# Optimization experiments

Hardware: AMD Instinct MI355X
Metric: run time of the kernel (lower is better)

## Reference

```python
import jax, jax.numpy as jnp
from jax import lax
import numpy as np

B, CIN, H, W = 32, 256, 56, 56
BOTTLE, GROWTH = 128, 32
EPS = 1e-5
QMAX = 127.0  # 8-bit symmetric


def _fq(x, scale, qmax=QMAX):
    # fake-quantize with straight-through estimator
    q = jnp.clip(jnp.round(x / scale), -qmax - 1.0, qmax) * scale
    return x + lax.stop_gradient(q - x)


def fake_quant_act(x):
    # per-tensor symmetric 8-bit activation quantization (QuantAct)
    scale = lax.stop_gradient(jnp.max(jnp.abs(x)) / QMAX + 1e-8)
    return _fq(x, scale), scale


def quant_weight_pc(w):
    # per-output-channel symmetric 8-bit weight quantization, w: [O,I,kh,kw]
    scale = lax.stop_gradient(jnp.max(jnp.abs(w), axis=(1, 2, 3)) / QMAX + 1e-8)
    return _fq(w, scale[:, None, None, None]), scale


def conv2d(x, w, pad):
    return lax.conv_general_dilated(
        x, w, window_strides=(1, 1), padding=[(pad, pad), (pad, pad)],
        dimension_numbers=("NCHW", "OIHW", "NCHW"))


def setup_inputs() -> dict:
    key = jax.random.key(0)
    ks = jax.random.split(key, 12)
    return {
        "batch": jax.random.normal(ks[0], (B, CIN, H, W), jnp.float32),
        "input_scaling_factor": jnp.float32(0.05),
        "bn1_gamma": jax.random.uniform(ks[1], (CIN,), jnp.float32, 0.5, 1.5),
        "bn1_beta": jax.random.normal(ks[2], (CIN,), jnp.float32) * 0.1,
        "bn1_mean": jax.random.normal(ks[3], (CIN,), jnp.float32) * 0.1,
        "bn1_var": jax.random.uniform(ks[4], (CIN,), jnp.float32, 0.5, 1.5),
        "conv1_w": jax.random.normal(ks[5], (BOTTLE, CIN, 1, 1), jnp.float32) * 0.05,
        "bn2_gamma": jax.random.uniform(ks[6], (BOTTLE,), jnp.float32, 0.5, 1.5),
        "bn2_beta": jax.random.normal(ks[7], (BOTTLE,), jnp.float32) * 0.1,
        "bn2_mean": jax.random.normal(ks[8], (BOTTLE,), jnp.float32) * 0.1,
        "bn2_var": jax.random.uniform(ks[9], (BOTTLE,), jnp.float32, 0.5, 1.5),
        "conv2_w": jax.random.normal(ks[10], (GROWTH, BOTTLE, 3, 3), jnp.float32) * 0.05,
    }


def reference(batch, input_scaling_factor, bn1_gamma, bn1_beta, bn1_mean,
              bn1_var, conv1_w, bn2_gamma, bn2_beta, bn2_mean, bn2_var,
              conv2_w):
    s_in = input_scaling_factor
    # ---- QuantBn1: BN with fake-quantized folded weight/bias ----
    w1 = bn1_gamma * lax.rsqrt(bn1_var + EPS)            # [CIN]
    b1 = bn1_beta - bn1_mean * w1                        # [CIN]
    s_bn = lax.stop_gradient(jnp.max(jnp.abs(w1)) / QMAX + 1e-8)
    w1q = _fq(w1, s_bn)
    b1q = _fq(b1, s_in * s_bn, qmax=2.0 ** 31)           # bias quantized at s_in*s_w
    x = batch * w1q[None, :, None, None] + b1q[None, :, None, None]
    x = jax.nn.relu(x)                                   # act1
    x, s_a1 = fake_quant_act(x)                          # quant_act1
    # ---- QuantBnConv2d: fold bn2 into conv1 (1x1), per-channel weight quant ----
    t = bn2_gamma * lax.rsqrt(bn2_var + EPS)             # [BOTTLE]
    wf = conv1_w * t[:, None, None, None]
    bf = bn2_beta - bn2_mean * t
    wfq, s_w1 = quant_weight_pc(wf)                      # s_w1: [BOTTLE]
    bfq = _fq(bf, s_a1 * s_w1, qmax=2.0 ** 31)
    x = conv2d(x, wfq, pad=0) + bfq[None, :, None, None]
    x = jax.nn.relu(x)                                   # act2
    x, s_a2 = fake_quant_act(x)                          # quant_act2
    # ---- QuantConv2d: 3x3 growth conv, per-channel weight quant ----
    w2q, s_w2 = quant_weight_pc(conv2_w)
    x = conv2d(x, w2q, pad=1)                            # [B, GROWTH, H, W]
    # ---- concat + output requant ----
    cat = jnp.concatenate([batch, x], axis=1)            # [B, CIN+GROWTH, H, W]
    out, s_out = fake_quant_act(cat)                     # quant_act_output
    return out, s_out
```

## Files before the change

kernel.cpp:

```cpp
#include <hip/hip_runtime.h>

typedef __attribute__((ext_vector_type(8))) short bf16x8;
typedef __attribute__((ext_vector_type(4))) float f32x4;

constexpr int B_   = 32;
constexpr int CIN  = 256;
constexpr int HW   = 56 * 56;
constexpr int BOT  = 128;
constexpr int GRW  = 32;
constexpr int COUT = CIN + GRW;
constexpr int NBATCH = B_ * CIN * HW;
constexpr int NX2    = B_ * BOT * HW;
constexpr int NOUT   = B_ * COUT * HW;

constexpr int NSLOT = 32;
constexpr int SSTR  = 32;
constexpr int OFF_SLOT = 16;
constexpr int OFF_W1Q  = OFF_SLOT + 4 * NSLOT * SSTR;
constexpr int OFF_B1Q  = OFF_W1Q + 256;
constexpr int OFF_BFQ  = OFF_B1Q + 256;
constexpr int OFF_SC1  = OFF_BFQ + 128;
constexpr int OFF_SC2  = OFF_SC1 + 128;
constexpr int OFF_WQ1B = OFF_SC2 + 32;
constexpr int OFF_W2B  = OFF_WQ1B + 16384;
constexpr int OFF_END  = OFF_W2B + 18432;
constexpr size_t X1Q_BYTE = (size_t)OFF_END * 4;
constexpr size_t X2_BYTE  = X1Q_BYTE + (size_t)NBATCH;
constexpr size_t X3_BYTE  = X2_BYTE + (size_t)NX2 * 4;
constexpr size_t X2B_BYTE = X3_BYTE + (size_t)(B_ * GRW * HW) * 4;

__device__ __forceinline__ void slotAtomicMax(float* ws, int a, int s, float v) {
    atomicMax((unsigned*)ws + OFF_SLOT + a * NSLOT * SSTR + s * SSTR, __float_as_uint(v));
}
__device__ __forceinline__ float slotMax(const float* ws, int a) {
    float m = 0.0f;
    #pragma unroll
    for (int s = 0; s < NSLOT; s++)
        m = fmaxf(m, ws[OFF_SLOT + a * NSLOT * SSTR + s * SSTR]);
    return m;
}

__device__ __forceinline__ float blockReduceMax256(float v) {
    #pragma unroll
    for (int o = 32; o > 0; o >>= 1) v = fmaxf(v, __shfl_down(v, o, 64));
    __shared__ float sm[4];
    if ((threadIdx.x & 63) == 0) sm[threadIdx.x >> 6] = v;
    __syncthreads();
    return fmaxf(fmaxf(sm[0], sm[1]), fmaxf(sm[2], sm[3]));
}
__device__ __forceinline__ float waveReduceMax(float v) {
    #pragma unroll
    for (int o = 32; o > 0; o >>= 1) v = fmaxf(v, __shfl_down(v, o, 64));
    return v;
}
__device__ __forceinline__ float clamp8(float r)   { return fminf(fmaxf(r, -128.0f), 127.0f); }
__device__ __forceinline__ float clampBig(float r) { return fminf(fmaxf(r, -2147483648.0f), 2147483648.0f); }
__device__ __forceinline__ unsigned short bf16u(float f) { return (unsigned short)(__float_as_uint(f) >> 16); }

__global__ void prep1_kernel(const float* __restrict__ g1, const float* __restrict__ b1p,
                             const float* __restrict__ m1, const float* __restrict__ v1,
                             const float* __restrict__ s_in_p, float* __restrict__ ws) {
    int c = threadIdx.x;
    unsigned* scal = (unsigned*)ws;
    for (int s = c; s < OFF_W1Q; s += 256) scal[s] = 0u;
    float s_in = *s_in_p;
    float r = 1.0f / sqrtf(v1[c] + 1e-5f);
    float w1 = __fmul_rn(g1[c], r);
    float b1 = __fsub_rn(b1p[c], __fmul_rn(m1[c], w1));
    float mx = blockReduceMax256(fabsf(w1));
    float s_bn = mx / 127.0f + 1e-8f;
    ws[OFF_W1Q + c] = __fmul_rn(clamp8(rintf(w1 / s_bn)), s_bn);
    float sb = __fmul_rn(s_in, s_bn);
    ws[OFF_B1Q + c] = __fmul_rn(clampBig(rintf(b1 / sb)), sb);
}

__global__ __launch_bounds__(256) void max1_kernel(const float4* __restrict__ batch4,
                                                   float* __restrict__ ws) {
    const float* w1q = ws + OFF_W1Q;
    const float* b1q = ws + OFF_B1Q;
    int tid = blockIdx.x * 256 + threadIdx.x;
    int row = tid >> 4;
    int f   = tid & 15;
    int c   = row & 255;
    float w = w1q[c], b = b1q[c];
    const float4* p = batch4 + (size_t)row * 784 + f;
    float mx1 = 0.0f, mxb = 0.0f;
    #pragma unroll 7
    for (int k = 0; k < 49; k++) {
        float4 v = p[k * 16];
        float x0 = fmaxf(__fadd_rn(__fmul_rn(v.x, w), b), 0.0f);
        float x1 = fmaxf(__fadd_rn(__fmul_rn(v.y, w), b), 0.0f);
        float x2 = fmaxf(__fadd_rn(__fmul_rn(v.z, w), b), 0.0f);
        float x3 = fmaxf(__fadd_rn(__fmul_rn(v.w, w), b), 0.0f);
        mx1 = fmaxf(mx1, fmaxf(fmaxf(x0, x1), fmaxf(x2, x3)));
        mxb = fmaxf(mxb, fmaxf(fmaxf(fabsf(v.x), fabsf(v.y)), fmaxf(fabsf(v.z), fabsf(v.w))));
    }
    mx1 = blockReduceMax256(mx1);
    __syncthreads();
    mxb = blockReduceMax256(mxb);
    if (threadIdx.x == 0) {
        int s = blockIdx.x & (NSLOT - 1);
        slotAtomicMax(ws, 0, s, mx1);
        slotAtomicMax(ws, 1, s, mxb);
    }
}

__global__ __launch_bounds__(256) void quant1_kernel(const float4* __restrict__ batch4,
                                                     float* __restrict__ ws) {
    __shared__ unsigned ldsq[256 * 17];
    const float* w1q = ws + OFF_W1Q;
    const float* b1q = ws + OFF_B1Q;
    float s_a1 = slotMax(ws, 0) / 127.0f + 1e-8f;
    int b = blockIdx.x / 49, hw0 = (blockIdx.x % 49) * 64;
    int t = threadIdx.x;
    int f = t & 15, cb = t >> 4;
    #pragma unroll
    for (int j = 0; j < 16; j++) {
        int c = cb + j * 16;
        float w = w1q[c], bb = b1q[c];
        float4 v = batch4[(b * 256 + c) * 784 + (hw0 >> 2) + f];
        unsigned q0 = (unsigned)(int)clamp8(rintf(fmaxf(__fadd_rn(__fmul_rn(v.x, w), bb), 0.0f) / s_a1));
        unsigned q1 = (unsigned)(int)clamp8(rintf(fmaxf(__fadd_rn(__fmul_rn(v.y, w), bb), 0.0f) / s_a1));
        unsigned q2 = (unsigned)(int)clamp8(rintf(fmaxf(__fadd_rn(__fmul_rn(v.z, w), bb), 0.0f) / s_a1));
        unsigned q3 = (unsigned)(int)clamp8(rintf(fmaxf(__fadd_rn(__fmul_rn(v.w, w), bb), 0.0f) / s_a1));
        ldsq[c * 17 + f] = q0 | (q1 << 8) | (q2 << 16) | (q3 << 24);
    }
    __syncthreads();
    const unsigned char* l8 = (const unsigned char*)ldsq;
    uint4* outv = (uint4*)((char*)ws + X1Q_BYTE);
    int hwl = t >> 2, cq = (t & 3) * 16;
    #pragma unroll
    for (int k = 0; k < 4; k++) {
        int c0 = cq + k * 64;
        unsigned u[4] = {0u, 0u, 0u, 0u};
        #pragma unroll
        for (int i = 0; i < 16; i++) {
            unsigned by = l8[(c0 + i) * 68 + hwl];
            u[i >> 2] |= by << ((i & 3) * 8);
        }
        uint4 val; val.x = u[0]; val.y = u[1]; val.z = u[2]; val.w = u[3];
        outv[(((size_t)b * 3136 + hw0 + hwl) * 256 + c0) >> 4] = val;
    }
}

__global__ void prep2_kernel(const float* __restrict__ c1w,
                             const float* __restrict__ g2, const float* __restrict__ b2,
                             const float* __restrict__ m2, const float* __restrict__ v2,
                             const float* __restrict__ c2w, float* __restrict__ ws) {
    int bi = blockIdx.x;
    int t = threadIdx.x;
    unsigned short* wq1b = (unsigned short*)(ws + OFF_WQ1B);
    unsigned short* w2b  = (unsigned short*)(ws + OFF_W2B);
    if (bi < BOT) {
        int o = bi;
        float tt = __fmul_rn(g2[o], 1.0f / sqrtf(v2[o] + 1e-5f));
        float wf = __fmul_rn(c1w[o * CIN + t], tt);
        float mx = blockReduceMax256(fabsf(wf));
        float s_w1 = mx / 127.0f + 1e-8f;
        float m = clamp8(rintf(wf / s_w1));
        wq1b[o * CIN + t] = bf16u(m);
        if (t == 0) {
            float s_a1 = slotMax(ws, 0) / 127.0f + 1e-8f;
            ws[OFF_SC1 + o] = __fmul_rn(s_a1, s_w1);
            float bf = __fsub_rn(b2[o], __fmul_rn(m2[o], tt));
            float sb = __fmul_rn(s_a1, s_w1);
            ws[OFF_BFQ + o] = __fmul_rn(clampBig(rintf(bf / sb)), sb);
        }
    } else {
        int g = bi - BOT;
        float mx = 0.0f;
        for (int s = t; s < BOT * 9; s += 256) mx = fmaxf(mx, fabsf(c2w[g * BOT * 9 + s]));
        mx = blockReduceMax256(mx);
        float s_w2 = mx / 127.0f + 1e-8f;
        for (int s = t; s < BOT * 9; s += 256) {
            int c = s / 9, tap = s - c * 9;
            float m = clamp8(rintf(c2w[g * BOT * 9 + s] / s_w2));
            w2b[(tap * GRW + g) * BOT + c] = bf16u(m);
        }
        if (t == 0) ws[OFF_SC2 + g] = s_w2;
    }
}

__global__ __launch_bounds__(256) void conv1_kernel(float* __restrict__ ws) {
    __shared__ unsigned short lA[64 * 136];
    __shared__ unsigned short lW[128 * 136];
    __shared__ float wred[4];
    const unsigned char* x1q = (const unsigned char*)((char*)ws + X1Q_BYTE);
    const unsigned short* wq1b = (const unsigned short*)(ws + OFF_WQ1B);
    const float* sc1 = ws + OFF_SC1;
    const float* bfq = ws + OFF_BFQ;
    float* x2 = (float*)((char*)ws + X2_BYTE);
    int b = blockIdx.x / 49, hw0 = (blockIdx.x % 49) * 64;
    int t = threadIdx.x, lane = t & 63, wv = t >> 6;
    int quad = lane >> 4, l16 = lane & 15;
    int mhalf = wv & 1, nhalf = wv >> 1;
    f32x4 acc[2][4];
    #pragma unroll
    for (int i = 0; i < 2; i++)
        #pragma unroll
        for (int j = 0; j < 4; j++) acc[i][j] = (f32x4){0.f, 0.f, 0.f, 0.f};

    for (int kc = 0; kc < 256; kc += 128) {
        __syncthreads();
        {
            int cb = t & 7, hwi = t >> 3;
            #pragma unroll
            for (int r = 0; r < 2; r++) {
                int hw = hwi + r * 32;
                uint4 p = *(const uint4*)(x1q + ((size_t)b * 3136 + hw0 + hw) * 256 + kc + cb * 16);
                unsigned wd[4] = {p.x, p.y, p.z, p.w};
                bf16x8 t0, t1;
                #pragma unroll
                for (int j = 0; j < 8; j++)
                    t0[j] = (short)bf16u((float)((wd[j >> 2] >> ((j & 3) * 8)) & 255u));
                #pragma unroll
                for (int j = 0; j < 8; j++)
                    t1[j] = (short)bf16u((float)((wd[2 + (j >> 2)] >> ((j & 3) * 8)) & 255u));
                *(bf16x8*)&lA[hw * 136 + cb * 16] = t0;
                *(bf16x8*)&lA[hw * 136 + cb * 16 + 8] = t1;
            }
        }
        {
            int cb = t & 7, oi = t >> 3;
            #pragma unroll
            for (int r = 0; r < 4; r++) {
                int o = oi + r * 32;
                uint4 p0 = *(const uint4*)(wq1b + o * 256 + kc + cb * 16);
                uint4 p1 = *(const uint4*)(wq1b + o * 256 + kc + cb * 16 + 8);
                *(uint4*)&lW[o * 136 + cb * 16] = p0;
                *(uint4*)&lW[o * 136 + cb * 16 + 8] = p1;
            }
        }
        __syncthreads();
        #pragma unroll
        for (int ks = 0; ks < 4; ks++) {
            bf16x8 a0 = *(const bf16x8*)&lA[(mhalf * 32 + l16) * 136 + ks * 32 + quad * 8];
            bf16x8 a1 = *(const bf16x8*)&lA[(mhalf * 32 + 16 + l16) * 136 + ks * 32 + quad * 8];
            #pragma unroll
            for (int nt = 0; nt < 4; nt++) {
                bf16x8 bfr = *(const bf16x8*)&lW[(nhalf * 64 + nt * 16 + l16) * 136 + ks * 32 + quad * 8];
                acc[0][nt] = __builtin_amdgcn_mfma_f32_16x16x32_bf16(a0, bfr, acc[0][nt], 0, 0, 0);
                acc[1][nt] = __builtin_amdgcn_mfma_f32_16x16x32_bf16(a1, bfr, acc[1][nt], 0, 0, 0);
            }
        }
    }
    float mx = 0.0f;
    #pragma unroll
    for (int nt = 0; nt < 4; nt++) {
        int o = nhalf * 64 + nt * 16 + l16;
        float s = sc1[o], bb = bfq[o];
        #pragma unroll
        for (int mt = 0; mt < 2; mt++) {
            int hw = hw0 + mhalf * 32 + mt * 16 + quad * 4;
            float4 v;
            v.x = fmaxf(__fadd_rn(__fmul_rn(acc[mt][nt][0], s), bb), 0.0f);
            v.y = fmaxf(__fadd_rn(__fmul_rn(acc[mt][nt][1], s), bb), 0.0f);
            v.z = fmaxf(__fadd_rn(__fmul_rn(acc[mt][nt][2], s), bb), 0.0f);
            v.w = fmaxf(__fadd_rn(__fmul_rn(acc[mt][nt][3], s), bb), 0.0f);
            mx = fmaxf(mx, fmaxf(fmaxf(v.x, v.y), fmaxf(v.z, v.w)));
            *(float4*)&x2[(size_t)(b * BOT + o) * HW + hw] = v;
        }
    }
    mx = waveReduceMax(mx);
    if (lane == 0) wred[wv] = mx;
    __syncthreads();
    if (t == 0) {
        float m = fmaxf(fmaxf(wred[0], wred[1]), fmaxf(wred[2], wred[3]));
        slotAtomicMax(ws, 2, blockIdx.x & (NSLOT - 1), m);
    }
}

__global__ __launch_bounds__(256) void quant2_kernel(float* __restrict__ ws) {
    __shared__ unsigned short lt[128 * 66];
    unsigned short* x2b = (unsigned short*)((char*)ws + X2B_BYTE);
    int b = blockIdx.x / 58, hp = blockIdx.x % 58;
    int t = threadIdx.x;
    uint4* dst = (uint4*)(x2b + (size_t)(b * 58 + hp) * 8192);
    if (hp == 0 || hp == 57) {
        uint4 z; z.x = z.y = z.z = z.w = 0u;
        #pragma unroll
        for (int k = 0; k < 4; k++) dst[t + k * 256] = z;
        return;
    }
    int h = hp - 1;
    float s_a2 = slotMax(ws, 2) / 127.0f + 1e-8f;
    float rinv = 1.0f / s_a2;
    const float4* x24 = (const float4*)((char*)ws + X2_BYTE);
    unsigned* ltw = (unsigned*)lt;
    int f = t & 15, cb = t >> 4;
    if (f < 14) {
        #pragma unroll
        for (int j = 0; j < 8; j++) {
            int c = cb + j * 16;
            float4 v = x24[((size_t)b * 128 + c) * 784 + h * 14 + f];
            unsigned q0 = bf16u(clamp8(rintf(v.x * rinv)));
            unsigned q1 = bf16u(clamp8(rintf(v.y * rinv)));
            unsigned q2 = bf16u(clamp8(rintf(v.z * rinv)));
            unsigned q3 = bf16u(clamp8(rintf(v.w * rinv)));
            ltw[c * 33 + f * 2]     = q0 | (q1 << 16);
            ltw[c * 33 + f * 2 + 1] = q2 | (q3 << 16);
        }
    }
    __syncthreads();
    #pragma unroll
    for (int k = 0; k < 4; k++) {
        int idx = t + k * 256;
        int cblk = idx & 15, wp = idx >> 4;
        unsigned u[4] = {0u, 0u, 0u, 0u};
        if (wp >= 1 && wp <= 56) {
            #pragma unroll
            for (int i = 0; i < 8; i++) {
                unsigned s = lt[(cblk * 8 + i) * 66 + (wp - 1)];
                u[i >> 1] |= s << ((i & 1) * 16);
            }
        }
        uint4 val; val.x = u[0]; val.y = u[1]; val.z = u[2]; val.w = u[3];
        dst[wp * 16 + cblk] = val;
    }
}

__global__ __launch_bounds__(256) void conv2_kernel(float* __restrict__ ws) {
    __shared__ unsigned short wt[9 * 32 * 40];
    __shared__ float wred[4];
    const unsigned short* x2b = (const unsigned short*)((char*)ws + X2B_BYTE);
    const unsigned short* w2b = (const unsigned short*)(ws + OFF_W2B);
    const float* sc2 = ws + OFF_SC2;
    float* x3 = (float*)((char*)ws + X3_BYTE);
    int b = blockIdx.x / 28, hg = blockIdx.x % 28;
    int t = threadIdx.x, lane = t & 63, wv = t >> 6;
    int quad = lane >> 4, l16 = lane & 15;
    int h = hg * 2 + (wv >> 1);
    int wq = wv & 1;
    int w0 = wq * 24;
    float s_a2 = slotMax(ws, 2) / 127.0f + 1e-8f;

    const unsigned short* rowp[2][3];
    #pragma unroll
    for (int mt = 0; mt < 2; mt++) {
        int w = w0 + mt * 16 + l16;
        #pragma unroll
        for (int dh = 0; dh < 3; dh++)
            rowp[mt][dh] = x2b + ((size_t)(b * 58 + h + dh) * 64 + w) * 128 + quad * 8;
    }
    f32x4 acc[2][2];
    #pragma unroll
    for (int i = 0; i < 2; i++) { acc[i][0] = (f32x4){0.f,0.f,0.f,0.f}; acc[i][1] = (f32x4){0.f,0.f,0.f,0.f}; }

    for (int cs = 0; cs < 4; cs++) {
        __syncthreads();
        for (int s = t; s < 1152; s += 256) {
            int gi = s >> 2, q = s & 3;
            *(uint4*)&wt[gi * 40 + q * 8] = *(const uint4*)(w2b + gi * 128 + cs * 32 + q * 8);
        }
        __syncthreads();
        #pragma unroll
        for (int tap = 0; tap < 9; tap++) {
            int dh = tap / 3, dw = tap % 3;
            bf16x8 b0 = *(const bf16x8*)&wt[(tap * 32 + l16) * 40 + quad * 8];
            bf16x8 b1 = *(const bf16x8*)&wt[(tap * 32 + 16 + l16) * 40 + quad * 8];
            #pragma unroll
            for (int mt = 0; mt < 2; mt++) {
                bf16x8 a = *(const bf16x8*)(rowp[mt][dh] + dw * 128 + cs * 32);
                acc[mt][0] = __builtin_amdgcn_mfma_f32_16x16x32_bf16(a, b0, acc[mt][0], 0, 0, 0);
                acc[mt][1] = __builtin_amdgcn_mfma_f32_16x16x32_bf16(a, b1, acc[mt][1], 0, 0, 0);
            }
        }
    }
    float mx = 0.0f;
    #pragma unroll
    for (int nt = 0; nt < 2; nt++) {
        int g = nt * 16 + l16;
        float s2 = __fmul_rn(s_a2, sc2[g]);
        #pragma unroll
        for (int mt = 0; mt < 2; mt++) {
            int wb = w0 + mt * 16 + quad * 4;
            if (wq == 0 || wb >= 32) {
                float4 v;
                v.x = __fmul_rn(acc[mt][nt][0], s2);
                v.y = __fmul_rn(acc[mt][nt][1], s2);
                v.z = __fmul_rn(acc[mt][nt][2], s2);
                v.w = __fmul_rn(acc[mt][nt][3], s2);
                mx = fmaxf(mx, fmaxf(fmaxf(fabsf(v.x), fabsf(v.y)), fmaxf(fabsf(v.z), fabsf(v.w))));
                *(float4*)&x3[(size_t)(b * GRW + g) * HW + h * 56 + wb] = v;
            }
        }
    }
    mx = waveReduceMax(mx);
    if (lane == 0) wred[wv] = mx;
    __syncthreads();
    if (t == 0) {
        float m = fmaxf(fmaxf(wred[0], wred[1]), fmaxf(wred[2], wred[3]));
        slotAtomicMax(ws, 3, blockIdx.x & (NSLOT - 1), m);
    }
}

__global__ __launch_bounds__(256) void outq_kernel(const float4* __restrict__ batch4,
                                                   const float* __restrict__ ws,
                                                   float* __restrict__ out) {
    const float4* x34 = (const float4*)((const char*)ws + X3_BYTE);
    float maxb = slotMax(ws, 1);
    float max3 = slotMax(ws, 3);
    float s_out = fmaxf(maxb, max3) / 127.0f + 1e-8f;
    float4* out4 = (float4*)out;
    int n4 = NOUT / 4;
    for (int i = blockIdx.x * blockDim.x + threadIdx.x; i < n4; i += gridDim.x * blockDim.x) {
        int chl = i / 784;
        int b = chl / COUT;
        int ch = chl - b * COUT;
        int hw4 = i - chl * 784;
        float4 v;
        if (ch < CIN) v = batch4[(b * CIN + ch) * 784 + hw4];
        else          v = x34[(b * GRW + (ch - CIN)) * 784 + hw4];
        float4 r;
        r.x = __fmul_rn(clamp8(rintf(v.x / s_out)), s_out);
        r.y = __fmul_rn(clamp8(rintf(v.y / s_out)), s_out);
        r.z = __fmul_rn(clamp8(rintf(v.z / s_out)), s_out);
        r.w = __fmul_rn(clamp8(rintf(v.w / s_out)), s_out);
        out4[i] = r;
    }
    if (blockIdx.x == 0 && threadIdx.x == 0) out[NOUT] = s_out;
}

extern "C" void kernel_launch(void* const* d_in, const int* in_sizes, int n_in,
                              void* d_out, int out_size, void* d_ws, size_t ws_size,
                              hipStream_t stream) {
    const float* batch = (const float*)d_in[0];
    const float* s_in  = (const float*)d_in[1];
    const float* g1    = (const float*)d_in[2];
    const float* b1    = (const float*)d_in[3];
    const float* m1    = (const float*)d_in[4];
    const float* v1    = (const float*)d_in[5];
    const float* c1w   = (const float*)d_in[6];
    const float* g2    = (const float*)d_in[7];
    const float* b2    = (const float*)d_in[8];
    const float* m2    = (const float*)d_in[9];
    const float* v2    = (const float*)d_in[10];
    const float* c2w   = (const float*)d_in[11];
    float* out = (float*)d_out;
    float* ws  = (float*)d_ws;

    hipLaunchKernelGGL(prep1_kernel, dim3(1), dim3(256), 0, stream, g1, b1, m1, v1, s_in, ws);
    hipLaunchKernelGGL(max1_kernel, dim3(512), dim3(256), 0, stream, (const float4*)batch, ws);
    hipLaunchKernelGGL(quant1_kernel, dim3(32 * 49), dim3(256), 0, stream, (const float4*)batch, ws);
    hipLaunchKernelGGL(prep2_kernel, dim3(160), dim3(256), 0, stream, c1w, g2, b2, m2, v2, c2w, ws);
    hipLaunchKernelGGL(conv1_kernel, dim3(32 * 49), dim3(256), 0, stream, ws);
    hipLaunchKernelGGL(quant2_kernel, dim3(32 * 58), dim3(256), 0, stream, ws);
    hipLaunchKernelGGL(conv2_kernel, dim3(32 * 28), dim3(256), 0, stream, ws);
    hipLaunchKernelGGL(outq_kernel, dim3(4096), dim3(256), 0, stream, (const float4*)batch, ws, out);
}
```

Measured before the change: 345.3 us.

## Fuse act2 quantization into conv2 loads and write padded NHWC fp32 from conv1

conv1 now writes its post-ReLU fp32 output directly into a zero-padded channels-last buffer, and a small kernel zeroes the halo. The separate quant2 pass that transposed and quantized x2 to bf16 is removed, and conv2 quantizes on the fly as it loads fp32 activations. This drops one kernel launch and a full read plus write of the intermediate. In exchange conv2 reads fp32 (twice the bytes of bf16) nine times per element through global memory, and conv1's stores become scattered scalar writes.

```diff
diff --git a/kernel.cpp b/kernel.cpp
--- a/kernel.cpp
+++ b/kernel.cpp
@@ -10,7 +10,6 @@
 constexpr int GRW  = 32;
 constexpr int COUT = CIN + GRW;
 constexpr int NBATCH = B_ * CIN * HW;
-constexpr int NX2    = B_ * BOT * HW;
 constexpr int NOUT   = B_ * COUT * HW;
 
 constexpr int NSLOT = 32;
@@ -25,9 +24,9 @@
 constexpr int OFF_W2B  = OFF_WQ1B + 16384;
 constexpr int OFF_END  = OFF_W2B + 18432;
 constexpr size_t X1Q_BYTE = (size_t)OFF_END * 4;
-constexpr size_t X2_BYTE  = X1Q_BYTE + (size_t)NBATCH;
-constexpr size_t X3_BYTE  = X2_BYTE + (size_t)NX2 * 4;
-constexpr size_t X2B_BYTE = X3_BYTE + (size_t)(B_ * GRW * HW) * 4;
+constexpr size_t X2F_BYTE = X1Q_BYTE + (size_t)NBATCH;
+constexpr size_t X2F_FLTS = (size_t)B_ * 58 * 64 * 128;
+constexpr size_t X3_BYTE  = X2F_BYTE + X2F_FLTS * 4;
 
 __device__ __forceinline__ void slotAtomicMax(float* ws, int a, int s, float v) {
     atomicMax((unsigned*)ws + OFF_SLOT + a * NSLOT * SSTR + s * SSTR, __float_as_uint(v));
@@ -72,6 +71,26 @@
     ws[OFF_W1Q + c] = __fmul_rn(clamp8(rintf(w1 / s_bn)), s_bn);
     float sb = __fmul_rn(s_in, s_bn);
     ws[OFF_B1Q + c] = __fmul_rn(clampBig(rintf(b1 / sb)), sb);
+}
+
+__global__ __launch_bounds__(256) void pad0_kernel(float* __restrict__ ws) {
+    float4* x2f4 = (float4*)((char*)ws + X2F_BYTE);
+    int b = blockIdx.x, t = threadIdx.x;
+    float4 z; z.x = z.y = z.z = z.w = 0.0f;
+    for (int i = t; i < 2 * 58 * 32; i += 256) {
+        int row  = i / (58 * 32);
+        int rest = i - row * (58 * 32);
+        int slot = rest >> 5, q = rest & 31;
+        int hp = row ? 57 : 0;
+        x2f4[(((size_t)(b * 58 + hp) * 64 + slot) * 128 >> 2) + q] = z;
+    }
+    for (int i = t; i < 56 * 2 * 32; i += 256) {
+        int hp   = 1 + (i >> 6);
+        int rest = i & 63;
+        int slot = (rest >> 5) ? 57 : 0;
+        int q = rest & 31;
+        x2f4[(((size_t)(b * 58 + hp) * 64 + slot) * 128 >> 2) + q] = z;
+    }
 }
 
 __global__ __launch_bounds__(256) void max1_kernel(const float4* __restrict__ batch4,
@@ -189,7 +208,7 @@
     const unsigned short* wq1b = (const unsigned short*)(ws + OFF_WQ1B);
     const float* sc1 = ws + OFF_SC1;
     const float* bfq = ws + OFF_BFQ;
-    float* x2 = (float*)((char*)ws + X2_BYTE);
+    float* x2f = (float*)((char*)ws + X2F_BYTE);
     int b = blockIdx.x / 49, hw0 = (blockIdx.x % 49) * 64;
     int t = threadIdx.x, lane = t & 63, wv = t >> 6;
     int quad = lane >> 4, l16 = lane & 15;
@@ -246,19 +265,24 @@
     }
     float mx = 0.0f;
     #pragma unroll
-    for (int nt = 0; nt < 4; nt++) {
-        int o = nhalf * 64 + nt * 16 + l16;
-        float s = sc1[o], bb = bfq[o];
-        #pragma unroll
-        for (int mt = 0; mt < 2; mt++) {
-            int hw = hw0 + mhalf * 32 + mt * 16 + quad * 4;
-            float4 v;
-            v.x = fmaxf(__fadd_rn(__fmul_rn(acc[mt][nt][0], s), bb), 0.0f);
-            v.y = fmaxf(__fadd_rn(__fmul_rn(acc[mt][nt][1], s), bb), 0.0f);
-            v.z = fmaxf(__fadd_rn(__fmul_rn(acc[mt][nt][2], s), bb), 0.0f);
-            v.w = fmaxf(__fadd_rn(__fmul_rn(acc[mt][nt][3], s), bb), 0.0f);
-            mx = fmaxf(mx, fmaxf(fmaxf(v.x, v.y), fmaxf(v.z, v.w)));
-            *(float4*)&x2[(size_t)(b * BOT + o) * HW + hw] = v;
+    for (int mt = 0; mt < 2; mt++) {
+        int hwg = hw0 + mhalf * 32 + mt * 16 + quad * 4;
+        int h = (int)(((unsigned)hwg * 9363u) >> 19);
+        int w = hwg - h * 56;
+        float* base0 = x2f + ((size_t)(b * 58 + h + 1) * 64 + (w + 1)) * 128;
+        #pragma unroll
+        for (int nt = 0; nt < 4; nt++) {
+            int o = nhalf * 64 + nt * 16 + l16;
+            float s = sc1[o], bb = bfq[o];
+            float v0 = fmaxf(__fadd_rn(__fmul_rn(acc[mt][nt][0], s), bb), 0.0f);
+            float v1 = fmaxf(__fadd_rn(__fmul_rn(acc[mt][nt][1], s), bb), 0.0f);
+            float v2 = fmaxf(__fadd_rn(__fmul_rn(acc[mt][nt][2], s), bb), 0.0f);
+            float v3 = fmaxf(__fadd_rn(__fmul_rn(acc[mt][nt][3], s), bb), 0.0f);
+            mx = fmaxf(mx, fmaxf(fmaxf(v0, v1), fmaxf(v2, v3)));
+            base0[o]       = v0;
+            base0[o + 128] = v1;
+            base0[o + 256] = v2;
+            base0[o + 384] = v3;
         }
     }
     mx = waveReduceMax(mx);
@@ -270,59 +294,10 @@
     }
 }
 
-__global__ __launch_bounds__(256) void quant2_kernel(float* __restrict__ ws) {
-    __shared__ unsigned short lt[128 * 66];
-    unsigned short* x2b = (unsigned short*)((char*)ws + X2B_BYTE);
-    int b = blockIdx.x / 58, hp = blockIdx.x % 58;
-    int t = threadIdx.x;
-    uint4* dst = (uint4*)(x2b + (size_t)(b * 58 + hp) * 8192);
-    if (hp == 0 || hp == 57) {
-        uint4 z; z.x = z.y = z.z = z.w = 0u;
-        #pragma unroll
-        for (int k = 0; k < 4; k++) dst[t + k * 256] = z;
-        return;
-    }
-    int h = hp - 1;
-    float s_a2 = slotMax(ws, 2) / 127.0f + 1e-8f;
-    float rinv = 1.0f / s_a2;
-    const float4* x24 = (const float4*)((char*)ws + X2_BYTE);
-    unsigned* ltw = (unsigned*)lt;
-    int f = t & 15, cb = t >> 4;
-    if (f < 14) {
-        #pragma unroll
-        for (int j = 0; j < 8; j++) {
-            int c = cb + j * 16;
-            float4 v = x24[((size_t)b * 128 + c) * 784 + h * 14 + f];
-            unsigned q0 = bf16u(clamp8(rintf(v.x * rinv)));
-            unsigned q1 = bf16u(clamp8(rintf(v.y * rinv)));
-            unsigned q2 = bf16u(clamp8(rintf(v.z * rinv)));
-            unsigned q3 = bf16u(clamp8(rintf(v.w * rinv)));
-            ltw[c * 33 + f * 2]     = q0 | (q1 << 16);
-            ltw[c * 33 + f * 2 + 1] = q2 | (q3 << 16);
-        }
-    }
-    __syncthreads();
-    #pragma unroll
-    for (int k = 0; k < 4; k++) {
-        int idx = t + k * 256;
-        int cblk = idx & 15, wp = idx >> 4;
-        unsigned u[4] = {0u, 0u, 0u, 0u};
-        if (wp >= 1 && wp <= 56) {
-            #pragma unroll
-            for (int i = 0; i < 8; i++) {
-                unsigned s = lt[(cblk * 8 + i) * 66 + (wp - 1)];
-                u[i >> 1] |= s << ((i & 1) * 16);
-            }
-        }
-        uint4 val; val.x = u[0]; val.y = u[1]; val.z = u[2]; val.w = u[3];
-        dst[wp * 16 + cblk] = val;
-    }
-}
-
 __global__ __launch_bounds__(256) void conv2_kernel(float* __restrict__ ws) {
     __shared__ unsigned short wt[9 * 32 * 40];
     __shared__ float wred[4];
-    const unsigned short* x2b = (const unsigned short*)((char*)ws + X2B_BYTE);
+    const float* x2f = (const float*)((char*)ws + X2F_BYTE);
     const unsigned short* w2b = (const unsigned short*)(ws + OFF_W2B);
     const float* sc2 = ws + OFF_SC2;
     float* x3 = (float*)((char*)ws + X3_BYTE);
@@ -333,14 +308,15 @@
     int wq = wv & 1;
     int w0 = wq * 24;
     float s_a2 = slotMax(ws, 2) / 127.0f + 1e-8f;
-
-    const unsigned short* rowp[2][3];
+    float rinv = 1.0f / s_a2;
+
+    const float* rowp[2][3];
     #pragma unroll
     for (int mt = 0; mt < 2; mt++) {
         int w = w0 + mt * 16 + l16;
         #pragma unroll
         for (int dh = 0; dh < 3; dh++)
-            rowp[mt][dh] = x2b + ((size_t)(b * 58 + h + dh) * 64 + w) * 128 + quad * 8;
+            rowp[mt][dh] = x2f + ((size_t)(b * 58 + h + dh) * 64 + w) * 128 + quad * 8;
     }
     f32x4 acc[2][2];
     #pragma unroll
@@ -360,7 +336,18 @@
             bf16x8 b1 = *(const bf16x8*)&wt[(tap * 32 + 16 + l16) * 40 + quad * 8];
             #pragma unroll
             for (int mt = 0; mt < 2; mt++) {
-                bf16x8 a = *(const bf16x8*)(rowp[mt][dh] + dw * 128 + cs * 32);
+                const float* p = rowp[mt][dh] + dw * 128 + cs * 32;
+                f32x4 u0 = *(const f32x4*)p;
+                f32x4 u1 = *(const f32x4*)(p + 4);
+                bf16x8 a;
+                a[0] = (short)bf16u(clamp8(rintf(u0[0] * rinv)));
+                a[1] = (short)bf16u(clamp8(rintf(u0[1] * rinv)));
+                a[2] = (short)bf16u(clamp8(rintf(u0[2] * rinv)));
+                a[3] = (short)bf16u(clamp8(rintf(u0[3] * rinv)));
+                a[4] = (short)bf16u(clamp8(rintf(u1[0] * rinv)));
+                a[5] = (short)bf16u(clamp8(rintf(u1[1] * rinv)));
+                a[6] = (short)bf16u(clamp8(rintf(u1[2] * rinv)));
+                a[7] = (short)bf16u(clamp8(rintf(u1[3] * rinv)));
                 acc[mt][0] = __builtin_amdgcn_mfma_f32_16x16x32_bf16(a, b0, acc[mt][0], 0, 0, 0);
                 acc[mt][1] = __builtin_amdgcn_mfma_f32_16x16x32_bf16(a, b1, acc[mt][1], 0, 0, 0);
             }
@@ -440,11 +427,11 @@
     float* ws  = (float*)d_ws;
 
     hipLaunchKernelGGL(prep1_kernel, dim3(1), dim3(256), 0, stream, g1, b1, m1, v1, s_in, ws);
+    hipLaunchKernelGGL(pad0_kernel, dim3(32), dim3(256), 0, stream, ws);
     hipLaunchKernelGGL(max1_kernel, dim3(512), dim3(256), 0, stream, (const float4*)batch, ws);
     hipLaunchKernelGGL(quant1_kernel, dim3(32 * 49), dim3(256), 0, stream, (const float4*)batch, ws);
     hipLaunchKernelGGL(prep2_kernel, dim3(160), dim3(256), 0, stream, c1w, g2, b2, m2, v2, c2w, ws);
     hipLaunchKernelGGL(conv1_kernel, dim3(32 * 49), dim3(256), 0, stream, ws);
-    hipLaunchKernelGGL(quant2_kernel, dim3(32 * 58), dim3(256), 0, stream, ws);
     hipLaunchKernelGGL(conv2_kernel, dim3(32 * 28), dim3(256), 0, stream, ws);
     hipLaunchKernelGGL(outq_kernel, dim3(4096), dim3(256), 0, stream, (const float4*)batch, ws, out);
 }
```

After: 365.1 us. +5.7%, slower.
